# Kernel tuning notes

Measured on AMD Instinct MI355X. Metric: run time of the kernel, lower is better.

## Reference

```python
import jax, jax.numpy as jnp
import numpy as np

N_QUBITS = 4
N_LAYERS = 2
BATCH = 524288


def _ry(theta):
    # RY(theta) = [[cos(t/2), -sin(t/2)], [sin(t/2), cos(t/2)]], shape [..., 2, 2]
    c = jnp.cos(theta / 2)
    s = jnp.sin(theta / 2)
    return jnp.stack([jnp.stack([c, -s], -1), jnp.stack([s, c], -1)], -2).astype(jnp.complex64)


def _rz(theta):
    # RZ(theta) = diag(exp(-i t/2), exp(i t/2))
    p = jnp.exp(-1j * theta / 2)
    pc = jnp.exp(1j * theta / 2)
    z = jnp.zeros_like(p)
    return jnp.stack([jnp.stack([p, z], -1), jnp.stack([z, pc], -1)], -2).astype(jnp.complex64)


def _apply_1q(state, gate, q):
    # state: [B,2,2,2,2] (axis 1+q is qubit q, wire 0 most significant as in default.qubit)
    # gate: [2,2] (shared) or [B,2,2] (per-sample)
    letters = list('abcd')
    t = letters[q]
    out = letters.copy()
    out[q] = 'z'
    if gate.ndim == 3:
        sub = f"Bz{t},B{''.join(letters)}->B{''.join(out)}"
    else:
        sub = f"z{t},B{''.join(letters)}->B{''.join(out)}"
    return jnp.einsum(sub, gate, state)


def _cnot(state, c, t):
    # flip target axis on the control=1 slice
    s0 = jnp.take(state, 0, axis=1 + c)
    s1 = jnp.take(state, 1, axis=1 + c)
    ta = 1 + t - (1 if t > c else 0)
    s1 = jnp.flip(s1, axis=ta)
    return jnp.stack([s0, s1], axis=1 + c)


def _circuit(x, weights):
    B = x.shape[0]
    state = jnp.zeros((B, 2, 2, 2, 2), jnp.complex64).at[:, 0, 0, 0, 0].set(1.0)
    ry_in = _ry(x)  # [B, 4, 2, 2], per-sample input encoding
    for q in range(N_QUBITS):
        state = _apply_1q(state, ry_in[:, q], q)
    for l in range(N_LAYERS):
        for q in range(N_QUBITS):
            state = _apply_1q(state, _rz(weights[l, q, 0]), q)
            state = _apply_1q(state, _ry(weights[l, q, 1]), q)
        for q in range(N_QUBITS - 1):
            state = _cnot(state, q, q + 1)
        state = _cnot(state, N_QUBITS - 1, 0)
    probs = jnp.abs(state.reshape(B, 16)) ** 2
    # <Z_i> = sum_s p(s) * (1 - 2*bit_i(s)); wire 0 is the most significant bit
    bits = (np.arange(16)[:, None] >> np.arange(N_QUBITS - 1, -1, -1)) & 1
    signs = jnp.asarray(1.0 - 2.0 * bits, jnp.float32)  # [16, 4]
    return probs @ signs  # [B, 4]


def setup_inputs() -> dict:
    key = jax.random.key(0)
    k1, k2 = jax.random.split(key)
    x = jax.random.normal(k1, (BATCH, N_QUBITS), dtype=jnp.float32)
    # TorchLayer default init: uniform in [0, 2*pi)
    weights = jax.random.uniform(k2, (N_LAYERS, N_QUBITS, 2), dtype=jnp.float32, minval=0.0, maxval=2 * np.pi)
    return {"x": x, "weights": weights}


def reference(x, weights):
    return _circuit(x, weights)
```

## Files before the change

### kernel.cpp

```cpp
#include <hip/hip_runtime.h>

#define BATCH 524288
#define TPB 256

typedef float vfloat16 __attribute__((ext_vector_type(16)));

__global__ void qprep_kernel(const float* __restrict__ w, float* __restrict__ ws) {
    const int tid = threadIdx.x;
    if (tid >= 16) return;

    float stx[16], sty[16];
    #pragma unroll
    for (int i = 0; i < 16; i++) { stx[i] = 0.f; sty[i] = 0.f; }
    stx[tid] = 1.f;

    #pragma unroll
    for (int l = 0; l < 2; l++) {
        #pragma unroll
        for (int q = 0; q < 4; q++) {
            const float tz = 0.5f * w[l * 8 + q * 2 + 0];
            const float ty = 0.5f * w[l * 8 + q * 2 + 1];
            const float cz = __cosf(tz), sz = __sinf(tz);
            const float cy = __cosf(ty), sy = __sinf(ty);
            const int mask = 8 >> q;
            #pragma unroll
            for (int i = 0; i < 16; i++) {
                float ax = stx[i], ay = sty[i];
                if (i & mask) { stx[i] = ax * cz - ay * sz; sty[i] = ay * cz + ax * sz; }
                else          { stx[i] = ax * cz + ay * sz; sty[i] = ay * cz - ax * sz; }
            }
            #pragma unroll
            for (int i = 0; i < 16; i++) {
                if (!(i & mask)) {
                    float a0x = stx[i], a0y = sty[i];
                    float a1x = stx[i | mask], a1y = sty[i | mask];
                    stx[i]        = cy * a0x - sy * a1x;
                    sty[i]        = cy * a0y - sy * a1y;
                    stx[i | mask] = sy * a0x + cy * a1x;
                    sty[i | mask] = sy * a0y + cy * a1y;
                }
            }
        }
        #pragma unroll
        for (int e = 0; e < 4; e++) {
            const int cqs[4] = {0, 1, 2, 3};
            const int tqs[4] = {1, 2, 3, 0};
            const int cm = 8 >> cqs[e];
            const int tm = 8 >> tqs[e];
            #pragma unroll
            for (int i = 0; i < 16; i++) {
                if ((i & cm) && !(i & tm)) {
                    float t0x = stx[i], t0y = sty[i];
                    stx[i] = stx[i | tm]; sty[i] = sty[i | tm];
                    stx[i | tm] = t0x;    sty[i | tm] = t0y;
                }
            }
        }
    }
    #pragma unroll
    for (int j = 0; j < 16; j++) {
        ws[j * 32 + tid]      = stx[j];
        ws[j * 32 + 16 + tid] = sty[j];
    }
}

__global__ __launch_bounds__(TPB, 4) void qmain_kernel(const float* __restrict__ x,
                                                       const float* __restrict__ U,
                                                       float* __restrict__ out) {
    const int base = blockIdx.x * TPB + threadIdx.x;

    const float4 xv = reinterpret_cast<const float4*>(x)[base];
    const float h0 = 0.5f * xv.x, h1 = 0.5f * xv.y, h2 = 0.5f * xv.z, h3 = 0.5f * xv.w;
    const float c0 = __cosf(h0), s0 = __sinf(h0);
    const float c1 = __cosf(h1), s1 = __sinf(h1);
    const float c2 = __cosf(h2), s2 = __sinf(h2);
    const float c3 = __cosf(h3), s3 = __sinf(h3);

    const float p01[4] = {c0 * c1, c0 * s1, s0 * c1, s0 * s1};
    const float p23[4] = {c2 * c3, c2 * s3, s2 * c3, s2 * s3};
    float sv[16];
    #pragma unroll
    for (int i = 0; i < 16; i++) sv[i] = p01[i >> 2] * p23[i & 3];

    float z0 = 0.f, z1 = 0.f, z2 = 0.f, z3 = 0.f;

    #pragma unroll
    for (int j = 0; j < 16; j++) {
        vfloat16 ur, ui;
        asm volatile("s_load_dwordx16 %0, %2, 0x0\n\t"
                     "s_load_dwordx16 %1, %2, 0x40\n\t"
                     "s_waitcnt lgkmcnt(0)"
                     : "=s"(ur), "=s"(ui)
                     : "s"(U + j * 32));
        float re = 0.f, im = 0.f;
        #pragma unroll
        for (int k = 0; k < 16; k++) {
            re = fmaf(ur[k], sv[k], re);
            im = fmaf(ui[k], sv[k], im);
        }
        const float p = re * re + im * im;
        z0 += (j & 8) ? -p : p;
        z1 += (j & 4) ? -p : p;
        z2 += (j & 2) ? -p : p;
        z3 += (j & 1) ? -p : p;
    }

    reinterpret_cast<float4*>(out)[base] = make_float4(z0, z1, z2, z3);
}

extern "C" void kernel_launch(void* const* d_in, const int* in_sizes, int n_in,
                              void* d_out, int out_size, void* d_ws, size_t ws_size,
                              hipStream_t stream) {
    const float* x = (const float*)d_in[0];
    const float* w = (const float*)d_in[1];
    float* out = (float*)d_out;
    float* U = (float*)d_ws;

    qprep_kernel<<<1, 64, 0, stream>>>(w, U);
    qmain_kernel<<<BATCH / TPB, TPB, 0, stream>>>(x, U, out);
}
```

Measured before the change: 71.69 us.

## Process four samples per thread and load two unitary rows per scalar fetch

Each thread now handles four batch samples, so every scalar-loaded row of the precomputed unitary is reused across four state vectors. Rows are fetched two at a time, which halves the number of scalar load and wait rounds. Launch bounds drop to two blocks per SM and the grid shrinks by a factor of four. The cost is more vector registers per thread and fewer waves in flight to hide memory latency.

Measured after the change: 73.69 us. 1.03x slower.

```diff
diff --git a/kernel.cpp b/kernel.cpp
--- a/kernel.cpp
+++ b/kernel.cpp
@@ -2,6 +2,7 @@
 
 #define BATCH 524288
 #define TPB 256
+#define V 4
 
 typedef float vfloat16 __attribute__((ext_vector_type(16)));
 
@@ -64,48 +65,68 @@
     }
 }
 
-__global__ __launch_bounds__(TPB, 4) void qmain_kernel(const float* __restrict__ x,
+__global__ __launch_bounds__(TPB, 2) void qmain_kernel(const float* __restrict__ x,
                                                        const float* __restrict__ U,
                                                        float* __restrict__ out) {
-    const int base = blockIdx.x * TPB + threadIdx.x;
+    const int base = blockIdx.x * (TPB * V) + threadIdx.x;
 
-    const float4 xv = reinterpret_cast<const float4*>(x)[base];
-    const float h0 = 0.5f * xv.x, h1 = 0.5f * xv.y, h2 = 0.5f * xv.z, h3 = 0.5f * xv.w;
-    const float c0 = __cosf(h0), s0 = __sinf(h0);
-    const float c1 = __cosf(h1), s1 = __sinf(h1);
-    const float c2 = __cosf(h2), s2 = __sinf(h2);
-    const float c3 = __cosf(h3), s3 = __sinf(h3);
+    float sv[V][16];
+    #pragma unroll
+    for (int v = 0; v < V; v++) {
+        const float4 xv = reinterpret_cast<const float4*>(x)[base + v * TPB];
+        const float h0 = 0.5f * xv.x, h1 = 0.5f * xv.y, h2 = 0.5f * xv.z, h3 = 0.5f * xv.w;
+        const float c0 = __cosf(h0), s0 = __sinf(h0);
+        const float c1 = __cosf(h1), s1 = __sinf(h1);
+        const float c2 = __cosf(h2), s2 = __sinf(h2);
+        const float c3 = __cosf(h3), s3 = __sinf(h3);
+        const float p01[4] = {c0 * c1, c0 * s1, s0 * c1, s0 * s1};
+        const float p23[4] = {c2 * c3, c2 * s3, s2 * c3, s2 * s3};
+        #pragma unroll
+        for (int i = 0; i < 16; i++) sv[v][i] = p01[i >> 2] * p23[i & 3];
+    }
 
-    const float p01[4] = {c0 * c1, c0 * s1, s0 * c1, s0 * s1};
-    const float p23[4] = {c2 * c3, c2 * s3, s2 * c3, s2 * s3};
-    float sv[16];
+    float z[V][4];
     #pragma unroll
-    for (int i = 0; i < 16; i++) sv[i] = p01[i >> 2] * p23[i & 3];
-
-    float z0 = 0.f, z1 = 0.f, z2 = 0.f, z3 = 0.f;
+    for (int v = 0; v < V; v++)
+        #pragma unroll
+        for (int i = 0; i < 4; i++) z[v][i] = 0.f;
 
     #pragma unroll
-    for (int j = 0; j < 16; j++) {
-        vfloat16 ur, ui;
-        asm volatile("s_load_dwordx16 %0, %2, 0x0\n\t"
-                     "s_load_dwordx16 %1, %2, 0x40\n\t"
+    for (int jj = 0; jj < 8; jj++) {
+        const int j0 = 2 * jj, j1 = 2 * jj + 1;
+        vfloat16 ur0, ui0, ur1, ui1;
+        asm volatile("s_load_dwordx16 %0, %4, 0x0\n\t"
+                     "s_load_dwordx16 %1, %4, 0x40\n\t"
+                     "s_load_dwordx16 %2, %4, 0x80\n\t"
+                     "s_load_dwordx16 %3, %4, 0xC0\n\t"
                      "s_waitcnt lgkmcnt(0)"
-                     : "=s"(ur), "=s"(ui)
-                     : "s"(U + j * 32));
-        float re = 0.f, im = 0.f;
+                     : "=s"(ur0), "=s"(ui0), "=s"(ur1), "=s"(ui1)
+                     : "s"(U + jj * 64));
         #pragma unroll
-        for (int k = 0; k < 16; k++) {
-            re = fmaf(ur[k], sv[k], re);
-            im = fmaf(ui[k], sv[k], im);
+        for (int v = 0; v < V; v++) {
+            float re0 = 0.f, im0 = 0.f, re1 = 0.f, im1 = 0.f;
+            #pragma unroll
+            for (int k = 0; k < 16; k++) {
+                const float s = sv[v][k];
+                re0 = fmaf(ur0[k], s, re0);
+                im0 = fmaf(ui0[k], s, im0);
+                re1 = fmaf(ur1[k], s, re1);
+                im1 = fmaf(ui1[k], s, im1);
+            }
+            const float p0 = fmaf(re0, re0, im0 * im0);
+            const float p1 = fmaf(re1, re1, im1 * im1);
+            z[v][0] += ((j0 & 8) ? -p0 : p0) + ((j1 & 8) ? -p1 : p1);
+            z[v][1] += ((j0 & 4) ? -p0 : p0) + ((j1 & 4) ? -p1 : p1);
+            z[v][2] += ((j0 & 2) ? -p0 : p0) + ((j1 & 2) ? -p1 : p1);
+            z[v][3] += ((j0 & 1) ? -p0 : p0) + ((j1 & 1) ? -p1 : p1);
         }
-        const float p = re * re + im * im;
-        z0 += (j & 8) ? -p : p;
-        z1 += (j & 4) ? -p : p;
-        z2 += (j & 2) ? -p : p;
-        z3 += (j & 1) ? -p : p;
     }
 
-    reinterpret_cast<float4*>(out)[base] = make_float4(z0, z1, z2, z3);
+    #pragma unroll
+    for (int v = 0; v < V; v++) {
+        reinterpret_cast<float4*>(out)[base + v * TPB] =
+            make_float4(z[v][0], z[v][1], z[v][2], z[v][3]);
+    }
 }
 
 extern "C" void kernel_launch(void* const* d_in, const int* in_sizes, int n_in,
@@ -117,5 +138,5 @@
     float* U = (float*)d_ws;
 
     qprep_kernel<<<1, 64, 0, stream>>>(w, U);
-    qmain_kernel<<<BATCH / TPB, TPB, 0, stream>>>(x, U, out);
+    qmain_kernel<<<BATCH / (TPB * V), TPB, 0, stream>>>(x, U, out);
 }
```
